# Optimization experiments

Hardware: AMD Instinct MI355X
Metric: run time of the kernel (lower is better)

Reference implementation:

```python
import jax, jax.numpy as jnp
import numpy as np

USER_NUM = 50000
ITEM_NUM = 100000
N = USER_NUM + ITEM_NUM
D = 64
NUM_LAYERS = 3          # len(hidden_units) in config
MAIN_LAYERS = NUM_LAYERS + 1  # forward() loops over hidden_units AFTER prepending embedding_dim
LMBD = 1e-4
SSL_TAU = 0.5
SSL_WEIGHT = 0.1
E = 2_000_000
E_KEEP = 1_800_000
EPS = 1e-12


def _edge_weights(src, dst, n):
    # calculate_graph: norm = out_degree^-0.5, edge_weight = norm[src]*norm[dst]
    deg = jnp.zeros((n,), jnp.float32).at[src].add(1.0)
    norm = jnp.power(jnp.maximum(deg, 1.0), -0.5)
    return norm[src] * norm[dst]


def setup_inputs() -> dict:
    key = jax.random.key(0)
    ks = jax.random.split(key, 12)
    user_emb = jax.random.normal(ks[0], (USER_NUM, D), jnp.float32) * 0.1
    item_emb = jax.random.normal(ks[1], (ITEM_NUM, D), jnp.float32) * 0.1
    src = jax.random.randint(ks[2], (E,), 0, N)
    dst = jax.random.randint(ks[3], (E,), 0, N)
    w = _edge_weights(src, dst, N)
    # augmented graphs (ED): random edge subset + self loops
    self_loop = jnp.arange(N, dtype=src.dtype)
    src1 = jnp.concatenate([jax.random.randint(ks[4], (E_KEEP - N,), 0, N) if E_KEEP - N > 0 else src[:0], jax.random.randint(ks[4], (E_KEEP - N,), 0, N)[:0], self_loop])
    src1 = jnp.concatenate([jax.random.randint(ks[4], (E_KEEP,), 0, N), self_loop])
    dst1 = jnp.concatenate([jax.random.randint(ks[5], (E_KEEP,), 0, N), self_loop])
    src1 = src1[: E_KEEP + N - 0]
    w1 = _edge_weights(src1, dst1, N)
    src2 = jnp.concatenate([jax.random.randint(ks[6], (E_KEEP,), 0, N), self_loop])
    dst2 = jnp.concatenate([jax.random.randint(ks[7], (E_KEEP,), 0, N), self_loop])
    w2 = _edge_weights(src2, dst2, N)
    user_id = jax.random.randint(ks[8], (4096,), 0, USER_NUM)
    item_id = jax.random.randint(ks[9], (4096,), 0, ITEM_NUM)
    neg_item_id = jax.random.randint(ks[10], (4096,), 0, ITEM_NUM)
    return {"user_emb": user_emb, "item_emb": item_emb, "src": src, "dst": dst, "w": w,
            "src1": src1, "dst1": dst1, "w1": w1, "src2": src2, "dst2": dst2, "w2": w2,
            "user_id": user_id, "item_id": item_id, "neg_item_id": neg_item_id}


def _l2norm(x):
    n = jnp.linalg.norm(x, axis=1, keepdims=True)
    return x / jnp.maximum(n, EPS)


def _propagate(user_emb, item_emb, src, dst, w, layers):
    # LightGCNConv per layer: m = h[src]*w; h' = scatter-sum to dst; L2 normalize
    u_list, i_list = [user_emb], [item_emb]
    u, i = user_emb, item_emb
    for _ in range(layers):
        h = jnp.concatenate([u, i], axis=0)            # [N, D]
        m = h[src] * w[:, None]                        # [E, D]
        h = jax.ops.segment_sum(m, dst, num_segments=N)
        h = _l2norm(h)
        u, i = h[:USER_NUM], h[USER_NUM:]
        u_list.append(u)
        i_list.append(i)
    fu = jnp.mean(jnp.stack(u_list, axis=1), axis=1)
    fi = jnp.mean(jnp.stack(i_list, axis=1), axis=1)
    return fu, fi


def reference(user_emb, item_emb, src, dst, w, src1, dst1, w1, src2, dst2, w2, user_id, item_id, neg_item_id):
    # main propagation (note: MAIN_LAYERS = NUM_LAYERS+1, faithful to the source bug)
    fu, fi = _propagate(user_emb, item_emb, src, dst, w, MAIN_LAYERS)
    ue = fu[user_id]
    pe = fi[item_id]
    ne = fi[neg_item_id]
    # BPR loss
    pos = jnp.sum(ue * pe, axis=1)
    neg = jnp.sum(ue * ne, axis=1)
    bpr = -jnp.mean(jax.nn.log_sigmoid(pos - neg))
    reg = (jnp.sum(ue ** 2) + jnp.sum(pe ** 2) + jnp.sum(ne ** 2)) / 2.0
    bpr_loss = bpr + LMBD * reg / ue.shape[0]
    # SSL loss on two augmented views (NUM_LAYERS layers each)
    u1, i1 = _propagate(user_emb, item_emb, src1, dst1, w1, NUM_LAYERS)
    u2, i2 = _propagate(user_emb, item_emb, src2, dst2, w2, NUM_LAYERS)
    ue1 = _l2norm(u1[user_id]); ue2 = _l2norm(u2[user_id]); au2 = _l2norm(u2)
    v1 = jnp.exp(jnp.sum(ue1 * ue2, axis=1) / SSL_TAU)
    v2 = jnp.sum(jnp.exp(ue1 @ au2.T / SSL_TAU), axis=1)
    ssl_user = -jnp.sum(jnp.log(v1 / v2))
    ie1 = _l2norm(i1[item_id]); ie2 = _l2norm(i2[item_id]); ai2 = _l2norm(i2)
    v3 = jnp.exp(jnp.sum(ie1 * ie2, axis=1) / SSL_TAU)
    v4 = jnp.sum(jnp.exp(ie1 @ ai2.T / SSL_TAU), axis=1)
    ssl_item = -jnp.sum(jnp.log(v3 / v4))
    ssl_loss = (ssl_item + ssl_user) * SSL_WEIGHT
    return bpr_loss + ssl_loss
```

## Files before the change

kernel.cpp:

```cpp
#include <hip/hip_runtime.h>
#include <math.h>
#include <stdint.h>

#define USER_NUM 50000
#define ITEM_NUM 100000
#define NN (USER_NUM + ITEM_NUM)
#define D 64
#define TAU_INV 2.0f
#define LMBD 0.0001f
#define NCITER 16
#define NBLK ((NN + 255) / 256)

typedef __bf16 bf16x8 __attribute__((ext_vector_type(8)));
typedef float  f32x4  __attribute__((ext_vector_type(4)));

static __device__ __forceinline__ unsigned short f2bf(float x) {
    union { float f; unsigned u; } v; v.f = x;
    unsigned r = v.u + 0x7FFFu + ((v.u >> 16) & 1u);
    return (unsigned short)(r >> 16);
}

__global__ void init_kernel(const float* __restrict__ ue, const float* __restrict__ ie,
                            float* __restrict__ h, float* __restrict__ acc) {
    int i = blockIdx.x * 256 + threadIdx.x;
    if (i < NN * D) {
        float v = (i < USER_NUM * D) ? ue[i] : ie[i - USER_NUM * D];
        h[i] = v; acc[i] = v;
    }
}

__global__ void deg_kernel(const int* __restrict__ dst, int* __restrict__ deg, int E) {
    int i = blockIdx.x * 256 + threadIdx.x;
    if (i < E) atomicAdd(&deg[dst[i]], 1);
}

__global__ void scan_reduce_kernel(const int* __restrict__ deg, int* __restrict__ bsum) {
    __shared__ int sd[256];
    int tid = threadIdx.x;
    int i = blockIdx.x * 256 + tid;
    sd[tid] = (i < NN) ? deg[i] : 0;
    __syncthreads();
    for (int o = 128; o; o >>= 1) { if (tid < o) sd[tid] += sd[tid + o]; __syncthreads(); }
    if (tid == 0) bsum[blockIdx.x] = sd[0];
}

__global__ void scan_mid_kernel(int* __restrict__ bsum, int* __restrict__ rowptr, int nblk) {
    __shared__ int sd[1024];
    int tid = threadIdx.x;
    int v = (tid < nblk) ? bsum[tid] : 0;
    sd[tid] = v;
    __syncthreads();
    for (int o = 1; o < 1024; o <<= 1) {
        int t = (tid >= o) ? sd[tid - o] : 0;
        __syncthreads();
        sd[tid] += t;
        __syncthreads();
    }
    if (tid < nblk) bsum[tid] = sd[tid] - v;
    if (tid == 0) rowptr[NN] = sd[1023];
}

__global__ void scan_final_kernel(const int* __restrict__ deg, const int* __restrict__ bsum,
                                  int* __restrict__ rowptr, int* __restrict__ cursor) {
    __shared__ int sd[256];
    int tid = threadIdx.x;
    int i = blockIdx.x * 256 + tid;
    int v = (i < NN) ? deg[i] : 0;
    sd[tid] = v;
    __syncthreads();
    for (int o = 1; o < 256; o <<= 1) {
        int t = (tid >= o) ? sd[tid - o] : 0;
        __syncthreads();
        sd[tid] += t;
        __syncthreads();
    }
    if (i < NN) {
        int ex = sd[tid] - v + bsum[blockIdx.x];
        rowptr[i] = ex;
        cursor[i] = ex;
    }
}

__global__ void fill_kernel(const int* __restrict__ src, const int* __restrict__ dst,
                            const float* __restrict__ w, int* __restrict__ cursor,
                            int2* __restrict__ perm, int E) {
    int i = blockIdx.x * 256 + threadIdx.x;
    if (i < E) {
        int p = atomicAdd(&cursor[dst[i]], 1);
        perm[p] = make_int2(src[i], __float_as_int(w[i]));
    }
}

__global__ __launch_bounds__(256) void gather_norm_kernel(const float* __restrict__ h,
        const int* __restrict__ rowptr, const int2* __restrict__ perm,
        float* __restrict__ hn, float* __restrict__ acc) {
    int gid = blockIdx.x * 256 + threadIdx.x;
    int row = gid >> 6;
    int lane = gid & 63;
    if (row >= NN) return;
    int beg = rowptr[row];
    int end = rowptr[row + 1];
    float s = 0.f;
    int e = beg;
    for (; e + 2 <= end; e += 2) {
        int2 p0 = perm[e];
        int2 p1 = perm[e + 1];
        float v0 = h[(size_t)p0.x * D + lane];
        float v1 = h[(size_t)p1.x * D + lane];
        s += v0 * __int_as_float(p0.y);
        s += v1 * __int_as_float(p1.y);
    }
    if (e < end) {
        int2 p0 = perm[e];
        s += h[(size_t)p0.x * D + lane] * __int_as_float(p0.y);
    }
    float q = s * s;
    #pragma unroll
    for (int o = 32; o; o >>= 1) q += __shfl_xor(q, o);
    float y = s / fmaxf(sqrtf(q), 1e-12f);
    size_t idx = (size_t)row * D + lane;
    hn[idx] = y;
    acc[idx] += y;
}

__global__ void norm_rows_bf_kernel(float* __restrict__ h, unsigned short* __restrict__ hb) {
    int gid = blockIdx.x * 256 + threadIdx.x;
    int row = gid >> 6;
    int lane = gid & 63;
    if (row >= NN) return;
    size_t idx = (size_t)row * D + lane;
    float x = h[idx];
    float s = x * x;
    #pragma unroll
    for (int o = 32; o; o >>= 1) s += __shfl_xor(s, o);
    float y = x / fmaxf(sqrtf(s), 1e-12f);
    h[idx] = y;
    hb[idx] = f2bf(y);
}

__global__ void bpr_kernel(const float* __restrict__ acc, const int* __restrict__ uid,
                           const int* __restrict__ iid, const int* __restrict__ nid,
                           float* __restrict__ scal, int B) {
    int gid = blockIdx.x * 256 + threadIdx.x;
    int r = gid >> 6;
    int lane = gid & 63;
    if (r >= B) return;
    const float inv = 1.0f / 5.0f;
    float ue = acc[(size_t)uid[r] * D + lane] * inv;
    float pe = acc[(size_t)(USER_NUM + iid[r]) * D + lane] * inv;
    float ne = acc[(size_t)(USER_NUM + nid[r]) * D + lane] * inv;
    float pos = ue * pe, neg = ue * ne, reg = ue * ue + pe * pe + ne * ne;
    #pragma unroll
    for (int o = 32; o; o >>= 1) {
        pos += __shfl_xor(pos, o);
        neg += __shfl_xor(neg, o);
        reg += __shfl_xor(reg, o);
    }
    if (lane == 0) {
        float x = pos - neg;
        float ls = (x >= 0.f) ? (-log1pf(expf(-x))) : (x - log1pf(expf(x)));
        atomicAdd(&scal[0], -ls);
        atomicAdd(&scal[1], reg * 0.5f);
    }
}

__global__ void extract_norm_kernel(const float* __restrict__ acc, const int* __restrict__ uid,
                                    const int* __restrict__ iid, unsigned short* __restrict__ ue1b,
                                    unsigned short* __restrict__ ie1b, int B) {
    int gid = blockIdx.x * 256 + threadIdx.x;
    int t = gid >> 6;
    int lane = gid & 63;
    if (t >= 2 * B) return;
    bool user = (t < B);
    int r = user ? t : (t - B);
    size_t srow = user ? (size_t)uid[r] * D : (size_t)(USER_NUM + iid[r]) * D;
    float x = acc[srow + lane];
    float s = x * x;
    #pragma unroll
    for (int o = 32; o; o >>= 1) s += __shfl_xor(s, o);
    float y = x / fmaxf(sqrtf(s), 1e-12f);
    (user ? ue1b : ie1b)[(size_t)r * D + lane] = f2bf(y);
}

__global__ __launch_bounds__(256) void ssl_mfma_kernel(const unsigned short* __restrict__ Ab,
                                                       const unsigned short* __restrict__ Bb,
                                                       float* __restrict__ rowsum, int M) {
    int wave = threadIdx.x >> 6;
    int lane = threadIdx.x & 63;
    int l15 = lane & 15;
    int lg  = lane >> 4;
    int rgbase = blockIdx.y * 64;
    int chunkbase = blockIdx.x * (128 * NCITER);

    bf16x8 afr[4][2];
    {
        const unsigned short* ab = Ab + (size_t)(rgbase + l15) * D + lg * 8;
        #pragma unroll
        for (int i = 0; i < 4; i++) {
            afr[i][0] = *(const bf16x8*)(ab + (size_t)i * 16 * D);
            afr[i][1] = *(const bf16x8*)(ab + (size_t)i * 16 * D + 32);
        }
    }

    float rowacc[4][4];
    #pragma unroll
    for (int i = 0; i < 4; i++)
        #pragma unroll
        for (int r = 0; r < 4; r++) rowacc[i][r] = 0.f;

    for (int it = 0; it < NCITER; it++) {
        int cb = chunkbase + it * 128 + wave * 32;
        bf16x8 bfr[2][2];
        bool val[2];
        #pragma unroll
        for (int cf = 0; cf < 2; cf++) {
            int col = cb + cf * 16 + l15;
            val[cf] = (col < M);
            int cc = val[cf] ? col : (M - 1);
            const unsigned short* bp = Bb + (size_t)cc * D + lg * 8;
            bfr[cf][0] = *(const bf16x8*)(bp);
            bfr[cf][1] = *(const bf16x8*)(bp + 32);
        }

        f32x4 acc[4][2];
        #pragma unroll
        for (int i = 0; i < 4; i++)
            #pragma unroll
            for (int cf = 0; cf < 2; cf++)
                acc[i][cf] = (f32x4){0.f, 0.f, 0.f, 0.f};

        #pragma unroll
        for (int i = 0; i < 4; i++) {
            #pragma unroll
            for (int cf = 0; cf < 2; cf++) {
                acc[i][cf] = __builtin_amdgcn_mfma_f32_16x16x32_bf16(afr[i][0], bfr[cf][0], acc[i][cf], 0, 0, 0);
                acc[i][cf] = __builtin_amdgcn_mfma_f32_16x16x32_bf16(afr[i][1], bfr[cf][1], acc[i][cf], 0, 0, 0);
            }
        }

        #pragma unroll
        for (int i = 0; i < 4; i++) {
            #pragma unroll
            for (int r = 0; r < 4; r++) {
                float e0 = val[0] ? __expf(TAU_INV * acc[i][0][r]) : 0.f;
                float e1 = val[1] ? __expf(TAU_INV * acc[i][1][r]) : 0.f;
                rowacc[i][r] += e0 + e1;
            }
        }
    }

    #pragma unroll
    for (int i = 0; i < 4; i++) {
        #pragma unroll
        for (int r = 0; r < 4; r++) {
            float s = rowacc[i][r];
            s += __shfl_xor(s, 1);
            s += __shfl_xor(s, 2);
            s += __shfl_xor(s, 4);
            s += __shfl_xor(s, 8);
            if (l15 == 0) atomicAdd(&rowsum[rgbase + i * 16 + lg * 4 + r], s);
        }
    }
}

__global__ void ssl_fin_kernel(const unsigned short* __restrict__ ue1b,
                               const unsigned short* __restrict__ ie1b,
                               const float* __restrict__ A2, const int* __restrict__ uid,
                               const int* __restrict__ iid, const float* __restrict__ rsU,
                               const float* __restrict__ rsI, float* __restrict__ scal, int B) {
    int gid = blockIdx.x * 256 + threadIdx.x;
    int t = gid >> 6;
    int lane = gid & 63;
    if (t >= 2 * B) return;
    bool user = (t < B);
    int r = user ? t : (t - B);
    const unsigned short* a = (user ? ue1b : ie1b) + (size_t)r * D;
    size_t brow = user ? (size_t)uid[r] * D : (size_t)(USER_NUM + iid[r]) * D;
    union { unsigned u; float f; } cv; cv.u = ((unsigned)a[lane]) << 16;
    float p = cv.f * A2[brow + lane];
    #pragma unroll
    for (int o = 32; o; o >>= 1) p += __shfl_xor(p, o);
    if (lane == 0) {
        float contrib = logf((user ? rsU : rsI)[r]) - p * TAU_INV;
        atomicAdd(&scal[user ? 2 : 3], contrib);
    }
}

__global__ void final_kernel(const float* __restrict__ scal, float* __restrict__ out, int B) {
    if (threadIdx.x == 0 && blockIdx.x == 0) {
        float invB = 1.0f / (float)B;
        float bpr_loss = scal[0] * invB + LMBD * scal[1] * invB;
        float ssl_loss = (scal[2] + scal[3]) * 0.1f;
        out[0] = bpr_loss + ssl_loss;
    }
}

extern "C" void kernel_launch(void* const* d_in, const int* in_sizes, int n_in,
                              void* d_out, int out_size, void* d_ws, size_t ws_size,
                              hipStream_t stream) {
    const float* user_emb = (const float*)d_in[0];
    const float* item_emb = (const float*)d_in[1];
    const int*   src  = (const int*)d_in[2];
    const int*   dst  = (const int*)d_in[3];
    const float* w    = (const float*)d_in[4];
    const int*   src1 = (const int*)d_in[5];
    const int*   dst1 = (const int*)d_in[6];
    const float* w1   = (const float*)d_in[7];
    const int*   src2 = (const int*)d_in[8];
    const int*   dst2 = (const int*)d_in[9];
    const float* w2   = (const float*)d_in[10];
    const int* user_id = (const int*)d_in[11];
    const int* item_id = (const int*)d_in[12];
    const int* neg_id  = (const int*)d_in[13];
    int E0 = in_sizes[2];
    int E1 = in_sizes[5];
    int E2 = in_sizes[8];
    int B  = in_sizes[11];

    size_t nd = (size_t)NN * D;
    float* hA  = (float*)d_ws;
    float* hB  = hA + nd;
    float* acc = hB + nd;
    float* ue1 = acc + nd;
    float* ie1 = ue1 + (size_t)B * D;
    float* rsU = ie1 + (size_t)B * D;
    float* rsI = rsU + B;
    float* scal = rsI + B;
    int* deg    = (int*)(scal + 8);
    int* rowptr = deg + NN;
    int* cursor = rowptr + NN + 1;
    int* bsum   = cursor + NN;
    int2* perm  = (int2*)(((uintptr_t)(bsum + NBLK) + 15) & ~(uintptr_t)15);
    unsigned short* ue1b = (unsigned short*)ue1;
    unsigned short* ie1b = (unsigned short*)ie1;
    unsigned short* bbuf = (unsigned short*)hA;

    hipMemsetAsync(rsU, 0, (size_t)(2 * B + 8) * sizeof(float), stream);

    int gridElem = (NN * D + 255) / 256;
    int gridRows = (NN * 64 + 255) / 256;

    auto propagate = [&](const int* s_, const int* d_, const float* w_, int E_, int layers) {
        hipMemsetAsync(deg, 0, (size_t)NN * sizeof(int), stream);
        int ge = (E_ + 255) / 256;
        deg_kernel<<<ge, 256, 0, stream>>>(d_, deg, E_);
        scan_reduce_kernel<<<NBLK, 256, 0, stream>>>(deg, bsum);
        scan_mid_kernel<<<1, 1024, 0, stream>>>(bsum, rowptr, NBLK);
        scan_final_kernel<<<NBLK, 256, 0, stream>>>(deg, bsum, rowptr, cursor);
        fill_kernel<<<ge, 256, 0, stream>>>(s_, d_, w_, cursor, perm, E_);
        init_kernel<<<gridElem, 256, 0, stream>>>(user_emb, item_emb, hA, acc);
        float* cur = hA;
        float* nxt = hB;
        for (int l = 0; l < layers; l++) {
            gather_norm_kernel<<<gridRows, 256, 0, stream>>>(cur, rowptr, perm, nxt, acc);
            float* t = cur; cur = nxt; nxt = t;
        }
    };

    propagate(src, dst, w, E0, 4);
    bpr_kernel<<<(B * 64) / 256, 256, 0, stream>>>(acc, user_id, item_id, neg_id, scal, B);

    propagate(src1, dst1, w1, E1, 3);
    extract_norm_kernel<<<(2 * B * 64) / 256, 256, 0, stream>>>(acc, user_id, item_id, ue1b, ie1b, B);

    propagate(src2, dst2, w2, E2, 3);
    norm_rows_bf_kernel<<<gridRows, 256, 0, stream>>>(acc, bbuf);

    {
        dim3 gu((USER_NUM + 128 * NCITER - 1) / (128 * NCITER), 64);
        ssl_mfma_kernel<<<gu, 256, 0, stream>>>(ue1b, bbuf, rsU, USER_NUM);
        dim3 gi((ITEM_NUM + 128 * NCITER - 1) / (128 * NCITER), 64);
        ssl_mfma_kernel<<<gi, 256, 0, stream>>>(ie1b, bbuf + (size_t)USER_NUM * D, rsI, ITEM_NUM);
    }

    ssl_fin_kernel<<<(2 * B * 64) / 256, 256, 0, stream>>>(ue1b, ie1b, acc, user_id, item_id,
                                                           rsU, rsI, scal, B);
    final_kernel<<<1, 64, 0, stream>>>(scal, (float*)d_out, B);
}
```

Baseline: 2.469 ms.

## Store propagated embeddings in bf16 and remap SSL grid for XCD locality

```diff
diff --git a/kernel.cpp b/kernel.cpp
--- a/kernel.cpp
+++ b/kernel.cpp
@@ -9,6 +9,7 @@
 #define TAU_INV 2.0f
 #define LMBD 0.0001f
 #define NCITER 16
+#define NRG 64
 #define NBLK ((NN + 255) / 256)
 
 typedef __bf16 bf16x8 __attribute__((ext_vector_type(8)));
@@ -19,13 +20,17 @@
     unsigned r = v.u + 0x7FFFu + ((v.u >> 16) & 1u);
     return (unsigned short)(r >> 16);
 }
+static __device__ __forceinline__ float bf2f(unsigned short b) {
+    union { unsigned u; float f; } v; v.u = ((unsigned)b) << 16;
+    return v.f;
+}
 
 __global__ void init_kernel(const float* __restrict__ ue, const float* __restrict__ ie,
-                            float* __restrict__ h, float* __restrict__ acc) {
+                            unsigned short* __restrict__ hb, float* __restrict__ acc) {
     int i = blockIdx.x * 256 + threadIdx.x;
     if (i < NN * D) {
         float v = (i < USER_NUM * D) ? ue[i] : ie[i - USER_NUM * D];
-        h[i] = v; acc[i] = v;
+        hb[i] = f2bf(v); acc[i] = v;
     }
 }
 
@@ -91,9 +96,9 @@
     }
 }
 
-__global__ __launch_bounds__(256) void gather_norm_kernel(const float* __restrict__ h,
+__global__ __launch_bounds__(256) void gather_norm_kernel(const unsigned short* __restrict__ hb,
         const int* __restrict__ rowptr, const int2* __restrict__ perm,
-        float* __restrict__ hn, float* __restrict__ acc) {
+        unsigned short* __restrict__ hn, float* __restrict__ acc) {
     int gid = blockIdx.x * 256 + threadIdx.x;
     int row = gid >> 6;
     int lane = gid & 63;
@@ -105,21 +110,21 @@
     for (; e + 2 <= end; e += 2) {
         int2 p0 = perm[e];
         int2 p1 = perm[e + 1];
-        float v0 = h[(size_t)p0.x * D + lane];
-        float v1 = h[(size_t)p1.x * D + lane];
+        float v0 = bf2f(hb[(size_t)p0.x * D + lane]);
+        float v1 = bf2f(hb[(size_t)p1.x * D + lane]);
         s += v0 * __int_as_float(p0.y);
         s += v1 * __int_as_float(p1.y);
     }
     if (e < end) {
         int2 p0 = perm[e];
-        s += h[(size_t)p0.x * D + lane] * __int_as_float(p0.y);
+        s += bf2f(hb[(size_t)p0.x * D + lane]) * __int_as_float(p0.y);
     }
     float q = s * s;
     #pragma unroll
     for (int o = 32; o; o >>= 1) q += __shfl_xor(q, o);
     float y = s / fmaxf(sqrtf(q), 1e-12f);
     size_t idx = (size_t)row * D + lane;
-    hn[idx] = y;
+    hn[idx] = f2bf(y);
     acc[idx] += y;
 }
 
@@ -184,13 +189,22 @@
 
 __global__ __launch_bounds__(256) void ssl_mfma_kernel(const unsigned short* __restrict__ Ab,
                                                        const unsigned short* __restrict__ Bb,
-                                                       float* __restrict__ rowsum, int M) {
+                                                       float* __restrict__ rowsum,
+                                                       int M, int nc) {
+    int bid = blockIdx.x;
+    int xcd = bid & 7;
+    int inner = bid >> 3;
+    int rg = inner & (NRG - 1);
+    int cgrp = inner >> 6;
+    int colChunk = cgrp * 8 + xcd;
+    if (colChunk >= nc) return;
+
     int wave = threadIdx.x >> 6;
     int lane = threadIdx.x & 63;
     int l15 = lane & 15;
     int lg  = lane >> 4;
-    int rgbase = blockIdx.y * 64;
-    int chunkbase = blockIdx.x * (128 * NCITER);
+    int rgbase = rg * 64;
+    int chunkbase = colChunk * (128 * NCITER);
 
     bf16x8 afr[4][2];
     {
@@ -276,8 +290,7 @@
     int r = user ? t : (t - B);
     const unsigned short* a = (user ? ue1b : ie1b) + (size_t)r * D;
     size_t brow = user ? (size_t)uid[r] * D : (size_t)(USER_NUM + iid[r]) * D;
-    union { unsigned u; float f; } cv; cv.u = ((unsigned)a[lane]) << 16;
-    float p = cv.f * A2[brow + lane];
+    float p = bf2f(a[lane]) * A2[brow + lane];
     #pragma unroll
     for (int o = 32; o; o >>= 1) p += __shfl_xor(p, o);
     if (lane == 0) {
@@ -318,22 +331,20 @@
     int B  = in_sizes[11];
 
     size_t nd = (size_t)NN * D;
-    float* hA  = (float*)d_ws;
-    float* hB  = hA + nd;
-    float* acc = hB + nd;
-    float* ue1 = acc + nd;
-    float* ie1 = ue1 + (size_t)B * D;
-    float* rsU = ie1 + (size_t)B * D;
-    float* rsI = rsU + B;
+    float* acc = (float*)d_ws;
+    unsigned short* hAb = (unsigned short*)(acc + nd);
+    unsigned short* hBb = hAb + nd;
+    unsigned short* ue1b = hBb + nd;
+    unsigned short* ie1b = ue1b + (size_t)B * D;
+    float* rsU  = (float*)(ie1b + (size_t)B * D);
+    float* rsI  = rsU + B;
     float* scal = rsI + B;
     int* deg    = (int*)(scal + 8);
     int* rowptr = deg + NN;
     int* cursor = rowptr + NN + 1;
     int* bsum   = cursor + NN;
     int2* perm  = (int2*)(((uintptr_t)(bsum + NBLK) + 15) & ~(uintptr_t)15);
-    unsigned short* ue1b = (unsigned short*)ue1;
-    unsigned short* ie1b = (unsigned short*)ie1;
-    unsigned short* bbuf = (unsigned short*)hA;
+    unsigned short* bbuf = hAb;
 
     hipMemsetAsync(rsU, 0, (size_t)(2 * B + 8) * sizeof(float), stream);
 
@@ -348,12 +359,12 @@
         scan_mid_kernel<<<1, 1024, 0, stream>>>(bsum, rowptr, NBLK);
         scan_final_kernel<<<NBLK, 256, 0, stream>>>(deg, bsum, rowptr, cursor);
         fill_kernel<<<ge, 256, 0, stream>>>(s_, d_, w_, cursor, perm, E_);
-        init_kernel<<<gridElem, 256, 0, stream>>>(user_emb, item_emb, hA, acc);
-        float* cur = hA;
-        float* nxt = hB;
+        init_kernel<<<gridElem, 256, 0, stream>>>(user_emb, item_emb, hAb, acc);
+        unsigned short* cur = hAb;
+        unsigned short* nxt = hBb;
         for (int l = 0; l < layers; l++) {
             gather_norm_kernel<<<gridRows, 256, 0, stream>>>(cur, rowptr, perm, nxt, acc);
-            float* t = cur; cur = nxt; nxt = t;
+            unsigned short* t = cur; cur = nxt; nxt = t;
         }
     };
 
@@ -367,10 +378,12 @@
     norm_rows_bf_kernel<<<gridRows, 256, 0, stream>>>(acc, bbuf);
 
     {
-        dim3 gu((USER_NUM + 128 * NCITER - 1) / (128 * NCITER), 64);
-        ssl_mfma_kernel<<<gu, 256, 0, stream>>>(ue1b, bbuf, rsU, USER_NUM);
-        dim3 gi((ITEM_NUM + 128 * NCITER - 1) / (128 * NCITER), 64);
-        ssl_mfma_kernel<<<gi, 256, 0, stream>>>(ie1b, bbuf + (size_t)USER_NUM * D, rsI, ITEM_NUM);
+        int ncU = (USER_NUM + 128 * NCITER - 1) / (128 * NCITER);
+        int gu = 8 * NRG * ((ncU + 7) / 8);
+        ssl_mfma_kernel<<<gu, 256, 0, stream>>>(ue1b, bbuf, rsU, USER_NUM, ncU);
+        int ncI = (ITEM_NUM + 128 * NCITER - 1) / (128 * NCITER);
+        int gi = 8 * NRG * ((ncI + 7) / 8);
+        ssl_mfma_kernel<<<gi, 256, 0, stream>>>(ie1b, bbuf + (size_t)USER_NUM * D, rsI, ITEM_NUM, ncI);
     }
 
     ssl_fin_kernel<<<(2 * B * 64) / 256, 256, 0, stream>>>(ue1b, ie1b, acc, user_id, item_id,
```

Result: faster. 2.401 ms (-2.8%).
